# Kernel optimization log

Measured on AMD Instinct MI355X. Metric: run time of the kernel, lower is better.

Reference implementation:

```python
import jax, jax.numpy as jnp
import numpy as np

B, T, L, D = 4, 64, 4096, 4096
MASK_VALUE = -1000000000.0


def setup_inputs() -> dict:
    key = jax.random.key(0)
    kq, km, ka = jax.random.split(key, 3)
    Q = jax.random.normal(kq, (1, T, D), dtype=jnp.float32)          # learned queries
    mask = jax.random.normal(km, (B, L, D), dtype=jnp.float32)       # acts as K and V
    attn_mask = jax.random.randint(ka, (B, T, L), 0, 2).astype(bool)  # True -> masked
    return {"mask": mask, "Q": Q, "attn_mask": attn_mask}


def reference(mask, Q, attn_mask):
    # scores: [B, T, L] = Q @ mask^T / sqrt(D)   (Q broadcast over batch)
    scale = 1.0 / np.sqrt(D).astype(np.float32)
    scores = jnp.einsum('td,bld->btl', Q[0], mask) * scale
    scores = jnp.where(attn_mask, MASK_VALUE, scores)
    attn = jax.nn.softmax(scores, axis=-1)
    # context: [B, T, D] = attn @ mask
    context = jnp.einsum('btl,bld->btd', attn, mask)
    return context
```

## Files before the change

### kernel.cpp

```cpp
#include <hip/hip_runtime.h>
#include <hip/hip_bf16.h>
#include <stdint.h>

#define B_ 4
#define T_ 64
#define L_ 4096
#define D_ 4096

using bf8   = __attribute__((ext_vector_type(8))) short;
using f32x4 = __attribute__((ext_vector_type(4))) float;

__device__ __forceinline__ unsigned short f2bf(float f) {
    union { float f; unsigned int u; } v;
    v.f = f;
    unsigned int r = v.u + 0x7fffu + ((v.u >> 16) & 1u);
    return (unsigned short)(r >> 16);
}

__device__ __forceinline__ int swz16(int row, int byteoff) {
    return byteoff ^ (((row ^ (row >> 3)) & 7) << 4);
}

__device__ __forceinline__ bf8 read_frag(const unsigned short* lds, int row, int kk, int lane) {
    int byte = kk * 64 + ((lane >> 4) << 4);
    int off  = row * 128 + swz16(row, byte);
    return *reinterpret_cast<const bf8*>(reinterpret_cast<const char*>(lds) + off);
}

__global__ __launch_bounds__(256, 1) void k_scores(
    const float* __restrict__ mask, const float* __restrict__ Q,
    float* __restrict__ scores) {
    __shared__ unsigned short lA[2][64 * 64];
    __shared__ unsigned short lB[2][64 * 64];
    const int tid  = threadIdx.x;
    const int lane = tid & 63;
    const int wave = tid >> 6;
    const int wm = wave >> 1, wn = wave & 1;
    const int b  = blockIdx.y;
    const int l0 = blockIdx.x * 64;
    const float* __restrict__ Mb = mask + (size_t)b * L_ * D_;

    f32x4 acc[2][2] = {};
    float4 ra[4], rb[4];

    auto loadTiles = [&](int k0) {
#pragma unroll
        for (int s = 0; s < 4; ++s) {
            int slot = tid + s * 256;
            int r = slot >> 4, c4 = slot & 15;
            ra[s] = *(reinterpret_cast<const float4*>(Q  + (size_t)r * D_ + k0) + c4);
            rb[s] = *(reinterpret_cast<const float4*>(Mb + (size_t)(l0 + r) * D_ + k0) + c4);
        }
    };
    auto writeTiles = [&](int buf) {
#pragma unroll
        for (int s = 0; s < 4; ++s) {
            int slot = tid + s * 256;
            int r = slot >> 4, c4 = slot & 15;
            int off = r * 128 + swz16(r, c4 * 8);
            ushort4 ua, ub;
            ua.x = f2bf(ra[s].x); ua.y = f2bf(ra[s].y); ua.z = f2bf(ra[s].z); ua.w = f2bf(ra[s].w);
            ub.x = f2bf(rb[s].x); ub.y = f2bf(rb[s].y); ub.z = f2bf(rb[s].z); ub.w = f2bf(rb[s].w);
            *reinterpret_cast<ushort4*>(reinterpret_cast<char*>(lA[buf]) + off) = ua;
            *reinterpret_cast<ushort4*>(reinterpret_cast<char*>(lB[buf]) + off) = ub;
        }
    };

    loadTiles(0);
    writeTiles(0);
    __syncthreads();
    const int NT = D_ / 64;
    for (int kt = 0; kt < NT; ++kt) {
        int cur = kt & 1;
        if (kt + 1 < NT) loadTiles((kt + 1) * 64);
#pragma unroll
        for (int kk = 0; kk < 2; ++kk) {
            bf8 a0 = read_frag(lA[cur], wm * 32 +      (lane & 15), kk, lane);
            bf8 a1 = read_frag(lA[cur], wm * 32 + 16 + (lane & 15), kk, lane);
            bf8 b0 = read_frag(lB[cur], wn * 32 +      (lane & 15), kk, lane);
            bf8 b1 = read_frag(lB[cur], wn * 32 + 16 + (lane & 15), kk, lane);
            acc[0][0] = __builtin_amdgcn_mfma_f32_16x16x32_bf16(a0, b0, acc[0][0], 0, 0, 0);
            acc[0][1] = __builtin_amdgcn_mfma_f32_16x16x32_bf16(a0, b1, acc[0][1], 0, 0, 0);
            acc[1][0] = __builtin_amdgcn_mfma_f32_16x16x32_bf16(a1, b0, acc[1][0], 0, 0, 0);
            acc[1][1] = __builtin_amdgcn_mfma_f32_16x16x32_bf16(a1, b1, acc[1][1], 0, 0, 0);
        }
        if (kt + 1 < NT) writeTiles(cur ^ 1);
        __syncthreads();
    }

    const int rgrp = (lane >> 4) * 4;
    const int cidx = lane & 15;
#pragma unroll
    for (int mi = 0; mi < 2; ++mi)
#pragma unroll
        for (int nj = 0; nj < 2; ++nj)
#pragma unroll
            for (int r = 0; r < 4; ++r) {
                int t = wm * 32 + mi * 16 + rgrp + r;
                int l = l0 + wn * 32 + nj * 16 + cidx;
                scores[((size_t)b * T_ + t) * L_ + l] = acc[mi][nj][r] * 0.015625f;
            }
}

__global__ __launch_bounds__(256, 4) void k_softmax(
    const float* __restrict__ scores, const int* __restrict__ am,
    unsigned short* __restrict__ attn) {
    const int row  = blockIdx.x;
    const int tid  = threadIdx.x;
    const int lane = tid & 63;
    const int wave = tid >> 6;
    const float* __restrict__ s = scores + (size_t)row * L_;
    const int*   __restrict__ m = am     + (size_t)row * L_;
    __shared__ float redmax[4], redsum[4];

    float v[16];
#pragma unroll
    for (int j = 0; j < 4; ++j) {
        float4 f = *(reinterpret_cast<const float4*>(s) + tid + j * 256);
        int4   q = *(reinterpret_cast<const int4*>(m)   + tid + j * 256);
        v[j * 4 + 0] = q.x ? -1.0e9f : f.x;
        v[j * 4 + 1] = q.y ? -1.0e9f : f.y;
        v[j * 4 + 2] = q.z ? -1.0e9f : f.z;
        v[j * 4 + 3] = q.w ? -1.0e9f : f.w;
    }
    float mx = -3.0e38f;
#pragma unroll
    for (int i = 0; i < 16; ++i) mx = fmaxf(mx, v[i]);
#pragma unroll
    for (int off = 32; off; off >>= 1) mx = fmaxf(mx, __shfl_xor(mx, off, 64));
    if (lane == 0) redmax[wave] = mx;
    __syncthreads();
    mx = fmaxf(fmaxf(redmax[0], redmax[1]), fmaxf(redmax[2], redmax[3]));

    float z = 0.f;
#pragma unroll
    for (int i = 0; i < 16; ++i) {
        v[i] = exp2f((v[i] - mx) * 1.4426950408889634f);
        z += v[i];
    }
#pragma unroll
    for (int off = 32; off; off >>= 1) z += __shfl_xor(z, off, 64);
    if (lane == 0) redsum[wave] = z;
    __syncthreads();
    z = (redsum[0] + redsum[1]) + (redsum[2] + redsum[3]);
    float inv = 1.0f / z;

    unsigned short* __restrict__ arow = attn + (size_t)row * L_;
#pragma unroll
    for (int j = 0; j < 4; ++j) {
        ushort4 u;
        u.x = f2bf(v[j * 4 + 0] * inv);
        u.y = f2bf(v[j * 4 + 1] * inv);
        u.z = f2bf(v[j * 4 + 2] * inv);
        u.w = f2bf(v[j * 4 + 3] * inv);
        *(reinterpret_cast<ushort4*>(arow) + tid + j * 256) = u;
    }
}

__global__ __launch_bounds__(256, 1) void k_context(
    const float* __restrict__ mask, const unsigned short* __restrict__ attn,
    float* __restrict__ out) {
    __shared__ unsigned short lA[2][64 * 64];
    __shared__ unsigned short lB[2][64 * 64];
    const int tid  = threadIdx.x;
    const int lane = tid & 63;
    const int wave = tid >> 6;
    const int wm = wave >> 1, wn = wave & 1;
    const int b  = blockIdx.y;
    const int d0 = blockIdx.x * 64;
    const float*          __restrict__ Mb = mask + (size_t)b * L_ * D_;
    const unsigned short* __restrict__ Ab = attn + (size_t)b * T_ * L_;

    f32x4 acc[2][2] = {};
    uint4  raA[2];
    float4 rbB[4];

    auto loadTiles = [&](int k0) {
#pragma unroll
        for (int s = 0; s < 2; ++s) {
            int slot = tid + s * 256;
            int r = slot >> 3, c8 = slot & 7;
            raA[s] = *(reinterpret_cast<const uint4*>(Ab + (size_t)r * L_ + k0) + c8);
        }
#pragma unroll
        for (int s = 0; s < 4; ++s) {
            int slot = tid + s * 256;
            int kl = slot >> 4, d4 = slot & 15;
            rbB[s] = *(reinterpret_cast<const float4*>(Mb + (size_t)(k0 + kl) * D_ + d0) + d4);
        }
    };
    auto writeTiles = [&](int buf) {
#pragma unroll
        for (int s = 0; s < 2; ++s) {
            int slot = tid + s * 256;
            int r = slot >> 3, c8 = slot & 7;
            int off = r * 128 + swz16(r, c8 * 16);
            *reinterpret_cast<uint4*>(reinterpret_cast<char*>(lA[buf]) + off) = raA[s];
        }
#pragma unroll
        for (int s = 0; s < 4; ++s) {
            int slot = tid + s * 256;
            int kl = slot >> 4, d4 = slot & 15;
            float fv[4] = { rbB[s].x, rbB[s].y, rbB[s].z, rbB[s].w };
#pragma unroll
            for (int i = 0; i < 4; ++i) {
                int d = d4 * 4 + i;
                int off = d * 128 + swz16(d, kl * 2);
                *reinterpret_cast<unsigned short*>(reinterpret_cast<char*>(lB[buf]) + off) = f2bf(fv[i]);
            }
        }
    };

    loadTiles(0);
    writeTiles(0);
    __syncthreads();
    const int NT = L_ / 64;
    for (int kt = 0; kt < NT; ++kt) {
        int cur = kt & 1;
        if (kt + 1 < NT) loadTiles((kt + 1) * 64);
#pragma unroll
        for (int kk = 0; kk < 2; ++kk) {
            bf8 a0 = read_frag(lA[cur], wm * 32 +      (lane & 15), kk, lane);
            bf8 a1 = read_frag(lA[cur], wm * 32 + 16 + (lane & 15), kk, lane);
            bf8 b0 = read_frag(lB[cur], wn * 32 +      (lane & 15), kk, lane);
            bf8 b1 = read_frag(lB[cur], wn * 32 + 16 + (lane & 15), kk, lane);
            acc[0][0] = __builtin_amdgcn_mfma_f32_16x16x32_bf16(a0, b0, acc[0][0], 0, 0, 0);
            acc[0][1] = __builtin_amdgcn_mfma_f32_16x16x32_bf16(a0, b1, acc[0][1], 0, 0, 0);
            acc[1][0] = __builtin_amdgcn_mfma_f32_16x16x32_bf16(a1, b0, acc[1][0], 0, 0, 0);
            acc[1][1] = __builtin_amdgcn_mfma_f32_16x16x32_bf16(a1, b1, acc[1][1], 0, 0, 0);
        }
        if (kt + 1 < NT) writeTiles(cur ^ 1);
        __syncthreads();
    }

    const int rgrp = (lane >> 4) * 4;
    const int cidx = lane & 15;
#pragma unroll
    for (int mi = 0; mi < 2; ++mi)
#pragma unroll
        for (int nj = 0; nj < 2; ++nj)
#pragma unroll
            for (int r = 0; r < 4; ++r) {
                int t = wm * 32 + mi * 16 + rgrp + r;
                int d = d0 + wn * 32 + nj * 16 + cidx;
                out[((size_t)b * T_ + t) * D_ + d] = acc[mi][nj][r];
            }
}

extern "C" void kernel_launch(void* const* d_in, const int* in_sizes, int n_in,
                              void* d_out, int out_size, void* d_ws, size_t ws_size,
                              hipStream_t stream) {
    const float* mask = (const float*)d_in[0];
    const float* Q    = (const float*)d_in[1];
    const int*   am   = (const int*)d_in[2];
    float* out = (float*)d_out;
    unsigned short* attn = (unsigned short*)d_ws;

    k_scores<<<dim3(L_ / 64, B_), 256, 0, stream>>>(mask, Q, out);
    k_softmax<<<dim3(B_ * T_), 256, 0, stream>>>(out, am, attn);
    k_context<<<dim3(D_ / 64, B_), 256, 0, stream>>>(mask, attn, out);
}
```

Before: 130.3 us.

## Double K-tile depth to 128 and pre-convert Q to bf16 once

The K-dimension tile in both GEMM kernels grows from 64 to 128, which halves the number of loop iterations and barriers and doubles the bytes in flight per stage. A small prep kernel converts Q to bf16 once into workspace, so k_scores loads bf16 Q directly and no longer repeats the fp32-to-bf16 conversion in every block. LDS use per block doubles and more registers are needed for the staged loads. The workspace must also hold the extra Q buffer.

```diff
diff --git a/kernel.cpp b/kernel.cpp
--- a/kernel.cpp
+++ b/kernel.cpp
@@ -23,15 +23,24 @@
 
 __device__ __forceinline__ bf8 read_frag(const unsigned short* lds, int row, int kk, int lane) {
     int byte = kk * 64 + ((lane >> 4) << 4);
-    int off  = row * 128 + swz16(row, byte);
+    int off  = row * 256 + swz16(row, byte);
     return *reinterpret_cast<const bf8*>(reinterpret_cast<const char*>(lds) + off);
 }
 
+__global__ __launch_bounds__(256) void k_qprep(const float* __restrict__ Q,
+                                               unsigned short* __restrict__ Qbf) {
+    int i = blockIdx.x * 256 + threadIdx.x;
+    float4 f = reinterpret_cast<const float4*>(Q)[i];
+    ushort4 u;
+    u.x = f2bf(f.x); u.y = f2bf(f.y); u.z = f2bf(f.z); u.w = f2bf(f.w);
+    reinterpret_cast<ushort4*>(Qbf)[i] = u;
+}
+
 __global__ __launch_bounds__(256, 1) void k_scores(
-    const float* __restrict__ mask, const float* __restrict__ Q,
+    const float* __restrict__ mask, const unsigned short* __restrict__ Qbf,
     float* __restrict__ scores) {
-    __shared__ unsigned short lA[2][64 * 64];
-    __shared__ unsigned short lB[2][64 * 64];
+    __shared__ unsigned short lA[2][64 * 128];
+    __shared__ unsigned short lB[2][64 * 128];
     const int tid  = threadIdx.x;
     const int lane = tid & 63;
     const int wave = tid >> 6;
@@ -41,40 +50,51 @@
     const float* __restrict__ Mb = mask + (size_t)b * L_ * D_;
 
     f32x4 acc[2][2] = {};
-    float4 ra[4], rb[4];
+    uint4  ra[4];
+    float4 rb[8];
 
     auto loadTiles = [&](int k0) {
 #pragma unroll
         for (int s = 0; s < 4; ++s) {
             int slot = tid + s * 256;
-            int r = slot >> 4, c4 = slot & 15;
-            ra[s] = *(reinterpret_cast<const float4*>(Q  + (size_t)r * D_ + k0) + c4);
-            rb[s] = *(reinterpret_cast<const float4*>(Mb + (size_t)(l0 + r) * D_ + k0) + c4);
+            int r = slot >> 4, c = slot & 15;
+            ra[s] = *reinterpret_cast<const uint4*>(Qbf + (size_t)r * D_ + k0 + c * 8);
+        }
+#pragma unroll
+        for (int s = 0; s < 8; ++s) {
+            int slot = tid + s * 256;
+            int r = slot >> 5, c = slot & 31;
+            rb[s] = *reinterpret_cast<const float4*>(Mb + (size_t)(l0 + r) * D_ + k0 + c * 4);
         }
     };
     auto writeTiles = [&](int buf) {
 #pragma unroll
         for (int s = 0; s < 4; ++s) {
             int slot = tid + s * 256;
-            int r = slot >> 4, c4 = slot & 15;
-            int off = r * 128 + swz16(r, c4 * 8);
-            ushort4 ua, ub;
-            ua.x = f2bf(ra[s].x); ua.y = f2bf(ra[s].y); ua.z = f2bf(ra[s].z); ua.w = f2bf(ra[s].w);
-            ub.x = f2bf(rb[s].x); ub.y = f2bf(rb[s].y); ub.z = f2bf(rb[s].z); ub.w = f2bf(rb[s].w);
-            *reinterpret_cast<ushort4*>(reinterpret_cast<char*>(lA[buf]) + off) = ua;
-            *reinterpret_cast<ushort4*>(reinterpret_cast<char*>(lB[buf]) + off) = ub;
+            int r = slot >> 4, c = slot & 15;
+            int off = r * 256 + swz16(r, c * 16);
+            *reinterpret_cast<uint4*>(reinterpret_cast<char*>(lA[buf]) + off) = ra[s];
+        }
+#pragma unroll
+        for (int s = 0; s < 8; ++s) {
+            int slot = tid + s * 256;
+            int r = slot >> 5, c = slot & 31;
+            int off = r * 256 + swz16(r, c * 8);
+            ushort4 u;
+            u.x = f2bf(rb[s].x); u.y = f2bf(rb[s].y); u.z = f2bf(rb[s].z); u.w = f2bf(rb[s].w);
+            *reinterpret_cast<ushort4*>(reinterpret_cast<char*>(lB[buf]) + off) = u;
         }
     };
 
     loadTiles(0);
     writeTiles(0);
     __syncthreads();
-    const int NT = D_ / 64;
+    const int NT = D_ / 128;
     for (int kt = 0; kt < NT; ++kt) {
         int cur = kt & 1;
-        if (kt + 1 < NT) loadTiles((kt + 1) * 64);
-#pragma unroll
-        for (int kk = 0; kk < 2; ++kk) {
+        if (kt + 1 < NT) loadTiles((kt + 1) * 128);
+#pragma unroll
+        for (int kk = 0; kk < 4; ++kk) {
             bf8 a0 = read_frag(lA[cur], wm * 32 +      (lane & 15), kk, lane);
             bf8 a1 = read_frag(lA[cur], wm * 32 + 16 + (lane & 15), kk, lane);
             bf8 b0 = read_frag(lB[cur], wn * 32 +      (lane & 15), kk, lane);
@@ -160,8 +180,8 @@
 __global__ __launch_bounds__(256, 1) void k_context(
     const float* __restrict__ mask, const unsigned short* __restrict__ attn,
     float* __restrict__ out) {
-    __shared__ unsigned short lA[2][64 * 64];
-    __shared__ unsigned short lB[2][64 * 64];
+    __shared__ unsigned short lA[2][64 * 128];
+    __shared__ unsigned short lB[2][64 * 128];
     const int tid  = threadIdx.x;
     const int lane = tid & 63;
     const int wave = tid >> 6;
@@ -172,40 +192,40 @@
     const unsigned short* __restrict__ Ab = attn + (size_t)b * T_ * L_;
 
     f32x4 acc[2][2] = {};
-    uint4  raA[2];
-    float4 rbB[4];
+    uint4  ra[4];
+    float4 rb[8];
 
     auto loadTiles = [&](int k0) {
 #pragma unroll
-        for (int s = 0; s < 2; ++s) {
-            int slot = tid + s * 256;
-            int r = slot >> 3, c8 = slot & 7;
-            raA[s] = *(reinterpret_cast<const uint4*>(Ab + (size_t)r * L_ + k0) + c8);
-        }
-#pragma unroll
-        for (int s = 0; s < 4; ++s) {
-            int slot = tid + s * 256;
-            int kl = slot >> 4, d4 = slot & 15;
-            rbB[s] = *(reinterpret_cast<const float4*>(Mb + (size_t)(k0 + kl) * D_ + d0) + d4);
+        for (int s = 0; s < 4; ++s) {
+            int slot = tid + s * 256;
+            int r = slot >> 4, c = slot & 15;
+            ra[s] = *reinterpret_cast<const uint4*>(Ab + (size_t)r * L_ + k0 + c * 8);
+        }
+#pragma unroll
+        for (int s = 0; s < 8; ++s) {
+            int slot = tid + s * 256;
+            int kl = slot >> 4, c = slot & 15;
+            rb[s] = *reinterpret_cast<const float4*>(Mb + (size_t)(k0 + kl) * D_ + d0 + c * 4);
         }
     };
     auto writeTiles = [&](int buf) {
 #pragma unroll
-        for (int s = 0; s < 2; ++s) {
-            int slot = tid + s * 256;
-            int r = slot >> 3, c8 = slot & 7;
-            int off = r * 128 + swz16(r, c8 * 16);
-            *reinterpret_cast<uint4*>(reinterpret_cast<char*>(lA[buf]) + off) = raA[s];
-        }
-#pragma unroll
-        for (int s = 0; s < 4; ++s) {
-            int slot = tid + s * 256;
-            int kl = slot >> 4, d4 = slot & 15;
-            float fv[4] = { rbB[s].x, rbB[s].y, rbB[s].z, rbB[s].w };
+        for (int s = 0; s < 4; ++s) {
+            int slot = tid + s * 256;
+            int r = slot >> 4, c = slot & 15;
+            int off = r * 256 + swz16(r, c * 16);
+            *reinterpret_cast<uint4*>(reinterpret_cast<char*>(lA[buf]) + off) = ra[s];
+        }
+#pragma unroll
+        for (int s = 0; s < 8; ++s) {
+            int slot = tid + s * 256;
+            int kl = slot >> 4, c = slot & 15;
+            float fv[4] = { rb[s].x, rb[s].y, rb[s].z, rb[s].w };
 #pragma unroll
             for (int i = 0; i < 4; ++i) {
-                int d = d4 * 4 + i;
-                int off = d * 128 + swz16(d, kl * 2);
+                int d = c * 4 + i;
+                int off = d * 256 + swz16(d, kl * 2);
                 *reinterpret_cast<unsigned short*>(reinterpret_cast<char*>(lB[buf]) + off) = f2bf(fv[i]);
             }
         }
@@ -214,12 +234,12 @@
     loadTiles(0);
     writeTiles(0);
     __syncthreads();
-    const int NT = L_ / 64;
+    const int NT = L_ / 128;
     for (int kt = 0; kt < NT; ++kt) {
         int cur = kt & 1;
-        if (kt + 1 < NT) loadTiles((kt + 1) * 64);
-#pragma unroll
-        for (int kk = 0; kk < 2; ++kk) {
+        if (kt + 1 < NT) loadTiles((kt + 1) * 128);
+#pragma unroll
+        for (int kk = 0; kk < 4; ++kk) {
             bf8 a0 = read_frag(lA[cur], wm * 32 +      (lane & 15), kk, lane);
             bf8 a1 = read_frag(lA[cur], wm * 32 + 16 + (lane & 15), kk, lane);
             bf8 b0 = read_frag(lB[cur], wn * 32 +      (lane & 15), kk, lane);
@@ -254,9 +274,12 @@
     const float* Q    = (const float*)d_in[1];
     const int*   am   = (const int*)d_in[2];
     float* out = (float*)d_out;
+
     unsigned short* attn = (unsigned short*)d_ws;
-
-    k_scores<<<dim3(L_ / 64, B_), 256, 0, stream>>>(mask, Q, out);
+    unsigned short* Qbf  = (unsigned short*)((char*)d_ws + (size_t)B_ * T_ * L_ * 2);
+
+    k_qprep<<<dim3(T_ * D_ / 4 / 256), 256, 0, stream>>>(Q, Qbf);
+    k_scores<<<dim3(L_ / 64, B_), 256, 0, stream>>>(mask, Qbf, out);
     k_softmax<<<dim3(B_ * T_), 256, 0, stream>>>(out, am, attn);
     k_context<<<dim3(D_ / 64, B_), 256, 0, stream>>>(mask, attn, out);
 }
```

After: 162.8 us. 1.25x slower.

## Deepen GEMM load pipeline, pre-convert Q to bf16, and simplify LDS swizzle

Applied to the files above, without the earlier changes.

Adds a small kernel that converts Q to bf16 once, so the scores kernel loads half as many Q bytes and skips per-tile conversion. Both GEMM kernels now keep two register stages of global loads in flight, pinned in place with sched_barrier and a custom barrier that waits only on LDS. Loads are reorganised so each thread covers one row in wider chunks, and the LDS swizzle is simplified. This costs an extra launch and more registers per thread, and the loop prefetches wrapped tiles at the end that are never used.

```diff
diff --git a/kernel.cpp b/kernel.cpp
--- a/kernel.cpp
+++ b/kernel.cpp
@@ -16,19 +16,87 @@
     unsigned int r = v.u + 0x7fffu + ((v.u >> 16) & 1u);
     return (unsigned short)(r >> 16);
 }
-
-__device__ __forceinline__ int swz16(int row, int byteoff) {
-    return byteoff ^ (((row ^ (row >> 3)) & 7) << 4);
-}
-
-__device__ __forceinline__ bf8 read_frag(const unsigned short* lds, int row, int kk, int lane) {
-    int byte = kk * 64 + ((lane >> 4) << 4);
-    int off  = row * 128 + swz16(row, byte);
-    return *reinterpret_cast<const bf8*>(reinterpret_cast<const char*>(lds) + off);
+__device__ __forceinline__ unsigned int pack2(float lo, float hi) {
+    return (unsigned int)f2bf(lo) | ((unsigned int)f2bf(hi) << 16);
+}
+
+__device__ __forceinline__ int tileOff(int row, int chunk) {
+    return row * 128 + ((chunk ^ (row & 7)) << 4);
+}
+
+__device__ __forceinline__ bf8 fragRead(const unsigned short* lds, int row, int kk, int lane) {
+    return *reinterpret_cast<const bf8*>(
+        reinterpret_cast<const char*>(lds) + tileOff(row, kk * 4 + (lane >> 4)));
+}
+
+__device__ __forceinline__ void pipe_barrier() {
+    asm volatile("s_waitcnt lgkmcnt(0)" ::: "memory");
+    __builtin_amdgcn_sched_barrier(0);
+    __builtin_amdgcn_s_barrier();
+    __builtin_amdgcn_sched_barrier(0);
+}
+
+__global__ __launch_bounds__(256) void k_qprep(const float* __restrict__ Q,
+                                               unsigned short* __restrict__ Qbf) {
+    int i = blockIdx.x * 256 + threadIdx.x;
+    float4 f = reinterpret_cast<const float4*>(Q)[i];
+    ushort4 u;
+    u.x = f2bf(f.x); u.y = f2bf(f.y); u.z = f2bf(f.z); u.w = f2bf(f.w);
+    reinterpret_cast<ushort4*>(Qbf)[i] = u;
+}
+
+
+struct SRegs { uint4 q[2]; float4 m[4]; };
+
+__device__ __forceinline__ void s_issue(SRegs& R, const unsigned short* Qb,
+                                        const float* Mb, int l0, int k0, int tid) {
+    const int r  = tid >> 2;
+    const int cq = (tid & 3) * 2;
+#pragma unroll
+    for (int s = 0; s < 2; ++s)
+        R.q[s] = *reinterpret_cast<const uint4*>(Qb + (size_t)r * D_ + k0 + (cq + s) * 8);
+    const int cm = (tid & 3) * 4;
+#pragma unroll
+    for (int s = 0; s < 4; ++s)
+        R.m[s] = *reinterpret_cast<const float4*>(Mb + (size_t)(l0 + r) * D_ + k0 + (cm + s) * 4);
+}
+
+__device__ __forceinline__ void s_commit(const SRegs& R, unsigned short* lA,
+                                         unsigned short* lB, int tid) {
+    const int r  = tid >> 2;
+    const int cq = (tid & 3) * 2;
+#pragma unroll
+    for (int s = 0; s < 2; ++s)
+        *reinterpret_cast<uint4*>(reinterpret_cast<char*>(lA) + tileOff(r, cq + s)) = R.q[s];
+    const int cm = (tid & 3) * 2;
+#pragma unroll
+    for (int j = 0; j < 2; ++j) {
+        uint4 w;
+        w.x = pack2(R.m[2 * j].x,     R.m[2 * j].y);
+        w.y = pack2(R.m[2 * j].z,     R.m[2 * j].w);
+        w.z = pack2(R.m[2 * j + 1].x, R.m[2 * j + 1].y);
+        w.w = pack2(R.m[2 * j + 1].z, R.m[2 * j + 1].w);
+        *reinterpret_cast<uint4*>(reinterpret_cast<char*>(lB) + tileOff(r, cm + j)) = w;
+    }
+}
+
+__device__ __forceinline__ void mfma_tile(const unsigned short* lA, const unsigned short* lB,
+                                          f32x4 acc[2][2], int wm, int wn, int lane) {
+#pragma unroll
+    for (int kk = 0; kk < 2; ++kk) {
+        bf8 a0 = fragRead(lA, wm * 32 +      (lane & 15), kk, lane);
+        bf8 a1 = fragRead(lA, wm * 32 + 16 + (lane & 15), kk, lane);
+        bf8 b0 = fragRead(lB, wn * 32 +      (lane & 15), kk, lane);
+        bf8 b1 = fragRead(lB, wn * 32 + 16 + (lane & 15), kk, lane);
+        acc[0][0] = __builtin_amdgcn_mfma_f32_16x16x32_bf16(a0, b0, acc[0][0], 0, 0, 0);
+        acc[0][1] = __builtin_amdgcn_mfma_f32_16x16x32_bf16(a0, b1, acc[0][1], 0, 0, 0);
+        acc[1][0] = __builtin_amdgcn_mfma_f32_16x16x32_bf16(a1, b0, acc[1][0], 0, 0, 0);
+        acc[1][1] = __builtin_amdgcn_mfma_f32_16x16x32_bf16(a1, b1, acc[1][1], 0, 0, 0);
+    }
 }
 
 __global__ __launch_bounds__(256, 1) void k_scores(
-    const float* __restrict__ mask, const float* __restrict__ Q,
+    const float* __restrict__ mask, const unsigned short* __restrict__ Qbf,
     float* __restrict__ scores) {
     __shared__ unsigned short lA[2][64 * 64];
     __shared__ unsigned short lB[2][64 * 64];
@@ -41,51 +109,27 @@
     const float* __restrict__ Mb = mask + (size_t)b * L_ * D_;
 
     f32x4 acc[2][2] = {};
-    float4 ra[4], rb[4];
-
-    auto loadTiles = [&](int k0) {
-#pragma unroll
-        for (int s = 0; s < 4; ++s) {
-            int slot = tid + s * 256;
-            int r = slot >> 4, c4 = slot & 15;
-            ra[s] = *(reinterpret_cast<const float4*>(Q  + (size_t)r * D_ + k0) + c4);
-            rb[s] = *(reinterpret_cast<const float4*>(Mb + (size_t)(l0 + r) * D_ + k0) + c4);
-        }
-    };
-    auto writeTiles = [&](int buf) {
-#pragma unroll
-        for (int s = 0; s < 4; ++s) {
-            int slot = tid + s * 256;
-            int r = slot >> 4, c4 = slot & 15;
-            int off = r * 128 + swz16(r, c4 * 8);
-            ushort4 ua, ub;
-            ua.x = f2bf(ra[s].x); ua.y = f2bf(ra[s].y); ua.z = f2bf(ra[s].z); ua.w = f2bf(ra[s].w);
-            ub.x = f2bf(rb[s].x); ub.y = f2bf(rb[s].y); ub.z = f2bf(rb[s].z); ub.w = f2bf(rb[s].w);
-            *reinterpret_cast<ushort4*>(reinterpret_cast<char*>(lA[buf]) + off) = ua;
-            *reinterpret_cast<ushort4*>(reinterpret_cast<char*>(lB[buf]) + off) = ub;
-        }
-    };
-
-    loadTiles(0);
-    writeTiles(0);
-    __syncthreads();
+    SRegs S0, S1;
     const int NT = D_ / 64;
-    for (int kt = 0; kt < NT; ++kt) {
-        int cur = kt & 1;
-        if (kt + 1 < NT) loadTiles((kt + 1) * 64);
-#pragma unroll
-        for (int kk = 0; kk < 2; ++kk) {
-            bf8 a0 = read_frag(lA[cur], wm * 32 +      (lane & 15), kk, lane);
-            bf8 a1 = read_frag(lA[cur], wm * 32 + 16 + (lane & 15), kk, lane);
-            bf8 b0 = read_frag(lB[cur], wn * 32 +      (lane & 15), kk, lane);
-            bf8 b1 = read_frag(lB[cur], wn * 32 + 16 + (lane & 15), kk, lane);
-            acc[0][0] = __builtin_amdgcn_mfma_f32_16x16x32_bf16(a0, b0, acc[0][0], 0, 0, 0);
-            acc[0][1] = __builtin_amdgcn_mfma_f32_16x16x32_bf16(a0, b1, acc[0][1], 0, 0, 0);
-            acc[1][0] = __builtin_amdgcn_mfma_f32_16x16x32_bf16(a1, b0, acc[1][0], 0, 0, 0);
-            acc[1][1] = __builtin_amdgcn_mfma_f32_16x16x32_bf16(a1, b1, acc[1][1], 0, 0, 0);
-        }
-        if (kt + 1 < NT) writeTiles(cur ^ 1);
-        __syncthreads();
+
+    s_issue(S0, Qbf, Mb, l0, 0, tid);
+    s_issue(S1, Qbf, Mb, l0, 64, tid);
+    s_commit(S0, lA[0], lB[0], tid);
+    pipe_barrier();
+
+    for (int kt = 0; kt < NT; kt += 2) {
+        int kA = (kt + 2 < NT ? kt + 2 : 0) * 64;
+        s_issue(S0, Qbf, Mb, l0, kA, tid);
+        __builtin_amdgcn_sched_barrier(0);
+        mfma_tile(lA[0], lB[0], acc, wm, wn, lane);
+        s_commit(S1, lA[1], lB[1], tid);
+        pipe_barrier();
+        int kB = (kt + 3 < NT ? kt + 3 : 0) * 64;
+        s_issue(S1, Qbf, Mb, l0, kB, tid);
+        __builtin_amdgcn_sched_barrier(0);
+        mfma_tile(lA[1], lB[1], acc, wm, wn, lane);
+        s_commit(S0, lA[0], lB[0], tid);
+        pipe_barrier();
     }
 
     const int rgrp = (lane >> 4) * 4;
@@ -154,6 +198,42 @@
         u.z = f2bf(v[j * 4 + 2] * inv);
         u.w = f2bf(v[j * 4 + 3] * inv);
         *(reinterpret_cast<ushort4*>(arow) + tid + j * 256) = u;
+    }
+}
+
+
+struct CRegs { uint4 a[2]; float4 m[4]; };
+
+__device__ __forceinline__ void c_issue(CRegs& R, const unsigned short* Ab,
+                                        const float* Mb, int d0, int k0, int tid) {
+    const int r  = tid >> 2;
+    const int ca = (tid & 3) * 2;
+#pragma unroll
+    for (int s = 0; s < 2; ++s)
+        R.a[s] = *reinterpret_cast<const uint4*>(Ab + (size_t)r * L_ + k0 + (ca + s) * 8);
+    const int cm = (tid & 3) * 4;
+#pragma unroll
+    for (int s = 0; s < 4; ++s)
+        R.m[s] = *reinterpret_cast<const float4*>(Mb + (size_t)(k0 + r) * D_ + d0 + (cm + s) * 4);
+}
+
+__device__ __forceinline__ void c_commit(const CRegs& R, unsigned short* lA,
+                                         unsigned short* lB, int tid) {
+    const int r  = tid >> 2;
+    const int ca = (tid & 3) * 2;
+#pragma unroll
+    for (int s = 0; s < 2; ++s)
+        *reinterpret_cast<uint4*>(reinterpret_cast<char*>(lA) + tileOff(r, ca + s)) = R.a[s];
+    const int db = (tid & 3) * 16;
+#pragma unroll
+    for (int s = 0; s < 4; ++s) {
+        float fv[4] = { R.m[s].x, R.m[s].y, R.m[s].z, R.m[s].w };
+#pragma unroll
+        for (int i = 0; i < 4; ++i) {
+            int d = db + s * 4 + i;
+            int off = d * 128 + ((((r >> 3) ^ (d & 7)) << 4)) + ((r & 7) << 1);
+            *reinterpret_cast<unsigned short*>(reinterpret_cast<char*>(lB) + off) = f2bf(fv[i]);
+        }
     }
 }
 
@@ -172,65 +252,27 @@
     const unsigned short* __restrict__ Ab = attn + (size_t)b * T_ * L_;
 
     f32x4 acc[2][2] = {};
-    uint4  raA[2];
-    float4 rbB[4];
-
-    auto loadTiles = [&](int k0) {
-#pragma unroll
-        for (int s = 0; s < 2; ++s) {
-            int slot = tid + s * 256;
-            int r = slot >> 3, c8 = slot & 7;
-            raA[s] = *(reinterpret_cast<const uint4*>(Ab + (size_t)r * L_ + k0) + c8);
-        }
-#pragma unroll
-        for (int s = 0; s < 4; ++s) {
-            int slot = tid + s * 256;
-            int kl = slot >> 4, d4 = slot & 15;
-            rbB[s] = *(reinterpret_cast<const float4*>(Mb + (size_t)(k0 + kl) * D_ + d0) + d4);
-        }
-    };
-    auto writeTiles = [&](int buf) {
-#pragma unroll
-        for (int s = 0; s < 2; ++s) {
-            int slot = tid + s * 256;
-            int r = slot >> 3, c8 = slot & 7;
-            int off = r * 128 + swz16(r, c8 * 16);
-            *reinterpret_cast<uint4*>(reinterpret_cast<char*>(lA[buf]) + off) = raA[s];
-        }
-#pragma unroll
-        for (int s = 0; s < 4; ++s) {
-            int slot = tid + s * 256;
-            int kl = slot >> 4, d4 = slot & 15;
-            float fv[4] = { rbB[s].x, rbB[s].y, rbB[s].z, rbB[s].w };
-#pragma unroll
-            for (int i = 0; i < 4; ++i) {
-                int d = d4 * 4 + i;
-                int off = d * 128 + swz16(d, kl * 2);
-                *reinterpret_cast<unsigned short*>(reinterpret_cast<char*>(lB[buf]) + off) = f2bf(fv[i]);
-            }
-        }
-    };
-
-    loadTiles(0);
-    writeTiles(0);
-    __syncthreads();
+    CRegs S0, S1;
     const int NT = L_ / 64;
-    for (int kt = 0; kt < NT; ++kt) {
-        int cur = kt & 1;
-        if (kt + 1 < NT) loadTiles((kt + 1) * 64);
-#pragma unroll
-        for (int kk = 0; kk < 2; ++kk) {
-            bf8 a0 = read_frag(lA[cur], wm * 32 +      (lane & 15), kk, lane);
-            bf8 a1 = read_frag(lA[cur], wm * 32 + 16 + (lane & 15), kk, lane);
-            bf8 b0 = read_frag(lB[cur], wn * 32 +      (lane & 15), kk, lane);
-            bf8 b1 = read_frag(lB[cur], wn * 32 + 16 + (lane & 15), kk, lane);
-            acc[0][0] = __builtin_amdgcn_mfma_f32_16x16x32_bf16(a0, b0, acc[0][0], 0, 0, 0);
-            acc[0][1] = __builtin_amdgcn_mfma_f32_16x16x32_bf16(a0, b1, acc[0][1], 0, 0, 0);
-            acc[1][0] = __builtin_amdgcn_mfma_f32_16x16x32_bf16(a1, b0, acc[1][0], 0, 0, 0);
-            acc[1][1] = __builtin_amdgcn_mfma_f32_16x16x32_bf16(a1, b1, acc[1][1], 0, 0, 0);
-        }
-        if (kt + 1 < NT) writeTiles(cur ^ 1);
-        __syncthreads();
+
+    c_issue(S0, Ab, Mb, d0, 0, tid);
+    c_issue(S1, Ab, Mb, d0, 64, tid);
+    c_commit(S0, lA[0], lB[0], tid);
+    pipe_barrier();
+
+    for (int kt = 0; kt < NT; kt += 2) {
+        int kA = (kt + 2 < NT ? kt + 2 : 0) * 64;
+        c_issue(S0, Ab, Mb, d0, kA, tid);
+        __builtin_amdgcn_sched_barrier(0);
+        mfma_tile(lA[0], lB[0], acc, wm, wn, lane);
+        c_commit(S1, lA[1], lB[1], tid);
+        pipe_barrier();
+        int kB = (kt + 3 < NT ? kt + 3 : 0) * 64;
+        c_issue(S1, Ab, Mb, d0, kB, tid);
+        __builtin_amdgcn_sched_barrier(0);
+        mfma_tile(lA[1], lB[1], acc, wm, wn, lane);
+        c_commit(S0, lA[0], lB[0], tid);
+        pipe_barrier();
     }
 
     const int rgrp = (lane >> 4) * 4;
@@ -254,9 +296,12 @@
     const float* Q    = (const float*)d_in[1];
     const int*   am   = (const int*)d_in[2];
     float* out = (float*)d_out;
+
     unsigned short* attn = (unsigned short*)d_ws;
-
-    k_scores<<<dim3(L_ / 64, B_), 256, 0, stream>>>(mask, Q, out);
+    unsigned short* Qbf  = (unsigned short*)((char*)d_ws + (size_t)B_ * T_ * L_ * 2);
+
+    k_qprep<<<dim3(T_ * D_ / 4 / 256), 256, 0, stream>>>(Q, Qbf);
+    k_scores<<<dim3(L_ / 64, B_), 256, 0, stream>>>(mask, Qbf, out);
     k_softmax<<<dim3(B_ * T_), 256, 0, stream>>>(out, am, attn);
     k_context<<<dim3(D_ / 64, B_), 256, 0, stream>>>(mask, attn, out);
 }
```

Measured after the change: 144.1 us. +10.6%, slower.
